# Kernel tuning notes

Measured on AMD Instinct MI355X. Metric: run time of the kernel, lower is better.

Reference implementation:

```python
import jax, jax.numpy as jnp
import numpy as np

N = 100000      # nodes
E = 3200000     # edges
G = 256         # graphs in batch
EPS = 1e-5      # BatchNorm eps


def gcn_conv(x, W, b, src, dst, norm):
    # x: [N, Fin] -> [N, Fout]. PyG GCNConv: linear, then sym-normalized
    # scatter-add over edges (self-loops already included in src/dst/norm).
    h = x @ W                                   # [N, Fout]
    msg = h[src] * norm[:, None]                # [E+N, Fout] gather + scale
    out = jax.ops.segment_sum(msg, dst, num_segments=N)
    return out + b


def bn_eval(x, gamma, beta, rm, rv):
    return (x - rm) * jax.lax.rsqrt(rv + EPS) * gamma + beta


def setup_inputs() -> dict:
    key = jax.random.key(0)
    ks = jax.random.split(key, 24)
    x = jax.random.normal(ks[0], (N, 8), dtype=jnp.float32)
    edge_index = jax.random.randint(ks[1], (2, E), 0, N, dtype=jnp.int64)
    batch = jnp.sort(jax.random.randint(ks[2], (N,), 0, G, dtype=jnp.int64))

    def lin(k, fin, fout):
        return jax.random.normal(k, (fin, fout), dtype=jnp.float32) / np.sqrt(fin)

    d = {
        "x": x, "edge_index": edge_index, "batch": batch,
        "W1": lin(ks[3], 8, 64),  "b1": jnp.zeros((64,), jnp.float32),
        "g1": jnp.ones((64,), jnp.float32), "be1": jnp.zeros((64,), jnp.float32),
        "rm1": jax.random.normal(ks[4], (64,), jnp.float32) * 0.1,
        "rv1": jnp.ones((64,), jnp.float32) + jax.random.uniform(ks[5], (64,)) * 0.1,
        "W2": lin(ks[6], 64, 64), "b2": jnp.zeros((64,), jnp.float32),
        "g2": jnp.ones((64,), jnp.float32), "be2": jnp.zeros((64,), jnp.float32),
        "rm2": jax.random.normal(ks[7], (64,), jnp.float32) * 0.1,
        "rv2": jnp.ones((64,), jnp.float32) + jax.random.uniform(ks[8], (64,)) * 0.1,
        "W3": lin(ks[9], 64, 64), "b3": jnp.zeros((64,), jnp.float32),
        "g3": jnp.ones((64,), jnp.float32), "be3": jnp.zeros((64,), jnp.float32),
        "rm3": jax.random.normal(ks[10], (64,), jnp.float32) * 0.1,
        "rv3": jnp.ones((64,), jnp.float32) + jax.random.uniform(ks[11], (64,)) * 0.1,
        "Wr1": lin(ks[12], 64, 64), "br1": jnp.zeros((64,), jnp.float32),
        "Wr2": lin(ks[13], 64, 2),  "br2": jnp.zeros((2,), jnp.float32),
    }
    return d


def reference(x, edge_index, batch,
              W1, b1, g1, be1, rm1, rv1,
              W2, b2, g2, be2, rm2, rv2,
              W3, b3, g3, be3, rm3, rv3,
              Wr1, br1, Wr2, br2):
    # add self-loops once; compute symmetric normalization deg^-1/2
    loops = jnp.arange(N, dtype=edge_index.dtype)
    src = jnp.concatenate([edge_index[0], loops])   # [E+N]
    dst = jnp.concatenate([edge_index[1], loops])
    deg = jax.ops.segment_sum(jnp.ones_like(dst, dtype=x.dtype), dst, num_segments=N)
    dinv = jnp.where(deg > 0, jax.lax.rsqrt(deg), 0.0)
    norm = dinv[src] * dinv[dst]                    # [E+N]

    h = jax.nn.relu(bn_eval(gcn_conv(x, W1, b1, src, dst, norm), g1, be1, rm1, rv1))
    h = jax.nn.relu(bn_eval(gcn_conv(h, W2, b2, src, dst, norm), g2, be2, rm2, rv2))
    h = jax.nn.relu(bn_eval(gcn_conv(h, W3, b3, src, dst, norm), g3, be3, rm3, rv3))

    # global mean pool over graph ids
    sums = jax.ops.segment_sum(h, batch, num_segments=G)           # [G, 64]
    cnts = jax.ops.segment_sum(jnp.ones((N,), h.dtype), batch, num_segments=G)
    pooled = sums / jnp.maximum(cnts, 1.0)[:, None]

    out = jax.nn.relu(pooled @ Wr1 + br1) @ Wr2 + br2              # [G, 2]
    return out
```

## Files before the change

### kernel.cpp

```cpp
#include <hip/hip_runtime.h>
#include <hip/hip_fp16.h>

#define NN 100000
#define NE 3200000
#define NG 256
#define NF (NN * 64)
#define FEPS 1e-5f
#define BSH 8
#define NB ((NN + 255) >> 8)
#define CHA 8192

static inline int ceil_div(int a, int b) { return (a + b - 1) / b; }


__global__ __launch_bounds__(256) void kA_hist(const int* __restrict__ dst,
                                               int* __restrict__ bh) {
    __shared__ int lh[NB];
    int t = threadIdx.x;
    for (int b = t; b < NB; b += 256) lh[b] = 0;
    __syncthreads();
    int e0 = blockIdx.x * CHA;
    int e1 = min(e0 + CHA, NE);
    for (int i = e0 + t; i < e1; i += 256) atomicAdd(&lh[dst[i] >> BSH], 1);
    __syncthreads();
    for (int b = t; b < NB; b += 256)
        if (lh[b]) atomicAdd(&bh[b], lh[b]);
}

__global__ __launch_bounds__(512) void kA_scan(const int* __restrict__ bh,
                                               int* __restrict__ bboff,
                                               int* __restrict__ bcur) {
    __shared__ int s[512];
    int t = threadIdx.x;
    int v = (t < NB) ? bh[t] : 0;
    s[t] = v;
    __syncthreads();
    for (int off = 1; off < 512; off <<= 1) {
        int add = (t >= off) ? s[t - off] : 0;
        __syncthreads();
        s[t] += add;
        __syncthreads();
    }
    if (t < NB) {
        int ex = s[t] - v;
        bboff[t] = ex;
        bcur[t] = ex;
    }
    if (t == 0) bboff[NB] = NE;
}

__global__ __launch_bounds__(256) void kA_fill(const int* __restrict__ src,
                                               const int* __restrict__ dst,
                                               int* __restrict__ bcur,
                                               int2* __restrict__ ebuf) {
    __shared__ int lh[NB];
    __shared__ int lbase[NB];
    __shared__ int lcur[NB];
    int t = threadIdx.x;
    for (int b = t; b < NB; b += 256) lh[b] = 0;
    __syncthreads();
    int e0 = blockIdx.x * CHA;
    int e1 = min(e0 + CHA, NE);
    for (int i = e0 + t; i < e1; i += 256) atomicAdd(&lh[dst[i] >> BSH], 1);
    __syncthreads();
    for (int b = t; b < NB; b += 256) {
        int c = lh[b];
        lbase[b] = c ? atomicAdd(&bcur[b], c) : 0;
        lcur[b] = 0;
    }
    __syncthreads();
    for (int i = e0 + t; i < e1; i += 256) {
        int d = dst[i];
        int s = src[i];
        int b = d >> BSH;
        int p = atomicAdd(&lcur[b], 1);
        ebuf[lbase[b] + p] = make_int2(s, d);
    }
}


__global__ __launch_bounds__(256) void kB_hist(const int2* __restrict__ ebuf,
                                               const int* __restrict__ bboff,
                                               int* __restrict__ cnt) {
    __shared__ int lc[256];
    int b = blockIdx.x;
    int t = threadIdx.x;
    lc[t] = 0;
    __syncthreads();
    int st = bboff[b], en = bboff[b + 1];
    for (int i = st + t; i < en; i += 256) atomicAdd(&lc[ebuf[i].y & 255], 1);
    __syncthreads();
    int node = (b << BSH) + t;
    if (node < NN) cnt[node] = lc[t];
}

__global__ __launch_bounds__(256) void k_dinv_xs(const int* __restrict__ cnt,
                                                 const float* __restrict__ x,
                                                 float* __restrict__ dinv,
                                                 __half* __restrict__ xs) {
    int i = blockIdx.x * 256 + threadIdx.x;
    if (i >= NN) return;
    float di = rsqrtf((float)cnt[i] + 1.0f);
    dinv[i] = di;
#pragma unroll
    for (int f = 0; f < 8; ++f) xs[i * 8 + f] = __float2half(x[i * 8 + f] * di);
}

__global__ __launch_bounds__(256) void k_scan1(const int* __restrict__ cnt,
                                               int* __restrict__ bsum) {
    __shared__ int s[256];
    int t = threadIdx.x;
    int i = blockIdx.x * 256 + t;
    s[t] = (i < NN) ? cnt[i] : 0;
    __syncthreads();
    for (int off = 128; off > 0; off >>= 1) {
        if (t < off) s[t] += s[t + off];
        __syncthreads();
    }
    if (t == 0) bsum[blockIdx.x] = s[0];
}

__global__ __launch_bounds__(512) void k_scan2(int* __restrict__ bsum, int nb) {
    __shared__ int s[512];
    int t = threadIdx.x;
    int v = (t < nb) ? bsum[t] : 0;
    s[t] = v;
    __syncthreads();
    for (int off = 1; off < 512; off <<= 1) {
        int add = (t >= off) ? s[t - off] : 0;
        __syncthreads();
        s[t] += add;
        __syncthreads();
    }
    if (t < nb) bsum[t] = s[t] - v;
}

__global__ __launch_bounds__(256) void k_scan3(const int* __restrict__ cnt,
                                               const int* __restrict__ bsum,
                                               int* __restrict__ rowptr) {
    __shared__ int s[256];
    int t = threadIdx.x;
    int i = blockIdx.x * 256 + t;
    int v = (i < NN) ? cnt[i] : 0;
    s[t] = v;
    __syncthreads();
    for (int off = 1; off < 256; off <<= 1) {
        int add = (t >= off) ? s[t - off] : 0;
        __syncthreads();
        s[t] += add;
        __syncthreads();
    }
    if (i < NN) rowptr[i] = s[t] - v + bsum[blockIdx.x];
}

__global__ __launch_bounds__(256) void kB_fill(const int2* __restrict__ ebuf,
                                               const int* __restrict__ bboff,
                                               const int* __restrict__ rowptr,
                                               int* __restrict__ csr) {
    __shared__ int rp[256];
    __shared__ int lc[256];
    int b = blockIdx.x;
    int t = threadIdx.x;
    int node = (b << BSH) + t;
    rp[t] = (node < NN) ? rowptr[node] : 0;
    lc[t] = 0;
    __syncthreads();
    int st = bboff[b], en = bboff[b + 1];
    for (int i = st + t; i < en; i += 256) {
        int2 e = ebuf[i];
        int dl = e.y & 255;
        int p = atomicAdd(&lc[dl], 1);
        csr[rp[dl] + p] = e.x;
    }
}


__global__ __launch_bounds__(256) void k_gxf8(const __half* __restrict__ xs,
                                              const int* __restrict__ rowptr,
                                              const int* __restrict__ cnt,
                                              const float* __restrict__ dinv,
                                              const int* __restrict__ csr,
                                              const float* __restrict__ W,
                                              const float* __restrict__ b,
                                              const float* __restrict__ g,
                                              const float* __restrict__ be,
                                              const float* __restrict__ rm,
                                              const float* __restrict__ rv,
                                              __half* __restrict__ out) {
    __shared__ float Ws[512];
    int tid = threadIdx.x;
    for (int i = tid; i < 512; i += 256) Ws[i] = W[i];
    __syncthreads();
    int wave = (blockIdx.x * 256 + tid) >> 6;
    int lane = tid & 63;
    if (wave >= NN) return;
    int es = lane >> 3, f = lane & 7;
    int st = rowptr[wave], n = cnt[wave];
    float acc = 0.f;
    for (int k0 = 0; k0 < n; k0 += 8) {
        int kk = k0 + es;
        if (kk < n) acc += __half2float(xs[csr[st + kk] * 8 + f]);
    }
    acc += __shfl_xor(acc, 8, 64);
    acc += __shfl_xor(acc, 16, 64);
    acc += __shfl_xor(acc, 32, 64);
    float di = dinv[wave];
    float pf = (acc + __half2float(xs[wave * 8 + f])) * di;
    float scale = g[lane] * rsqrtf(rv[lane] + FEPS);
    float shift = be[lane] + (b[lane] - rm[lane]) * scale;
    float o = 0.f;
#pragma unroll
    for (int k = 0; k < 8; ++k)
        o = fmaf(__shfl(pf, k, 64), Ws[k * 64 + lane], o);
    o = fmaxf(fmaf(o, scale, shift), 0.f);
    out[wave * 64 + lane] = __float2half(o * di);
}

template <bool SCALE_OUT>
__global__ __launch_bounds__(256) void k_gxf64(const __half* __restrict__ Hin,
                                               const int* __restrict__ rowptr,
                                               const int* __restrict__ cnt,
                                               const float* __restrict__ dinv,
                                               const int* __restrict__ csr,
                                               const float* __restrict__ W,
                                               const float* __restrict__ b,
                                               const float* __restrict__ g,
                                               const float* __restrict__ be,
                                               const float* __restrict__ rm,
                                               const float* __restrict__ rv,
                                               __half* __restrict__ out) {
    __shared__ float Ws[4096];
    int tid = threadIdx.x;
    for (int i = tid; i < 4096; i += 256) Ws[i] = W[i];
    __syncthreads();
    int wave = (blockIdx.x * 256 + tid) >> 6;
    int lane = tid & 63;
    if (wave >= NN) return;
    int st = rowptr[wave], n = cnt[wave];
    float a0 = __half2float(Hin[wave * 64 + lane]);
    float a1 = 0.f;
    int k = 0;
    while (k < n) {
        int rem = n - k;
        int chunk = rem < 64 ? rem : 64;
        int eidx = (lane < chunk) ? csr[st + k + lane] : 0;
        int j = 0;
        for (; j + 8 <= chunk; j += 8) {
            int s0 = __shfl(eidx, j + 0, 64);
            int s1 = __shfl(eidx, j + 1, 64);
            int s2 = __shfl(eidx, j + 2, 64);
            int s3 = __shfl(eidx, j + 3, 64);
            int s4 = __shfl(eidx, j + 4, 64);
            int s5 = __shfl(eidx, j + 5, 64);
            int s6 = __shfl(eidx, j + 6, 64);
            int s7 = __shfl(eidx, j + 7, 64);
            float v0 = __half2float(Hin[s0 * 64 + lane]);
            float v1 = __half2float(Hin[s1 * 64 + lane]);
            float v2 = __half2float(Hin[s2 * 64 + lane]);
            float v3 = __half2float(Hin[s3 * 64 + lane]);
            float v4 = __half2float(Hin[s4 * 64 + lane]);
            float v5 = __half2float(Hin[s5 * 64 + lane]);
            float v6 = __half2float(Hin[s6 * 64 + lane]);
            float v7 = __half2float(Hin[s7 * 64 + lane]);
            a0 += (v0 + v1) + (v2 + v3);
            a1 += (v4 + v5) + (v6 + v7);
        }
        for (; j < chunk; ++j) {
            int s = __shfl(eidx, j, 64);
            a0 += __half2float(Hin[s * 64 + lane]);
        }
        k += chunk;
    }
    float di = dinv[wave];
    float pf = (a0 + a1) * di;
    float scale = g[lane] * rsqrtf(rv[lane] + FEPS);
    float shift = be[lane] + (b[lane] - rm[lane]) * scale;
    float o0 = 0.f, o1 = 0.f, o2 = 0.f, o3 = 0.f;
#pragma unroll
    for (int k2 = 0; k2 < 64; k2 += 4) {
        o0 = fmaf(__shfl(pf, k2 + 0, 64), Ws[(k2 + 0) * 64 + lane], o0);
        o1 = fmaf(__shfl(pf, k2 + 1, 64), Ws[(k2 + 1) * 64 + lane], o1);
        o2 = fmaf(__shfl(pf, k2 + 2, 64), Ws[(k2 + 2) * 64 + lane], o2);
        o3 = fmaf(__shfl(pf, k2 + 3, 64), Ws[(k2 + 3) * 64 + lane], o3);
    }
    float o = (o0 + o1) + (o2 + o3);
    o = fmaxf(fmaf(o, scale, shift), 0.f);
    if (SCALE_OUT) o *= di;
    out[wave * 64 + lane] = __float2half(o);
}


__global__ __launch_bounds__(256) void k_pool(const __half* __restrict__ h,
                                              const int* __restrict__ batch,
                                              float* __restrict__ sums,
                                              float* __restrict__ cnts) {
    const int CHUNK = 32;
    int gw = (blockIdx.x * 256 + threadIdx.x) >> 6;
    int lane = threadIdx.x & 63;
    int nw = (gridDim.x * 256) >> 6;
    int nchunks = (NN + CHUNK - 1) / CHUNK;
    for (int c = gw; c < nchunks; c += nw) {
        int n0 = c * CHUNK;
        int n1 = min(n0 + CHUNK, NN);
        int gcur = batch[n0];
        float accf = 0.f;
        float cntf = 0.f;
        for (int n = n0; n < n1; ++n) {
            int gg = batch[n];
            if (gg != gcur) {
                atomicAdd(&sums[gcur * 64 + lane], accf);
                if (lane == 0) atomicAdd(&cnts[gcur], cntf);
                accf = 0.f;
                cntf = 0.f;
                gcur = gg;
            }
            accf += __half2float(h[n * 64 + lane]);
            cntf += 1.f;
        }
        atomicAdd(&sums[gcur * 64 + lane], accf);
        if (lane == 0) atomicAdd(&cnts[gcur], cntf);
    }
}

__global__ __launch_bounds__(256) void k_head(const float* __restrict__ sums,
                                              const float* __restrict__ cnts,
                                              const float* __restrict__ Wr1,
                                              const float* __restrict__ br1,
                                              const float* __restrict__ Wr2,
                                              const float* __restrict__ br2,
                                              float* __restrict__ out) {
    int wave = (blockIdx.x * 256 + threadIdx.x) >> 6;
    int lane = threadIdx.x & 63;
    if (wave >= NG) return;
    float c = fmaxf(cnts[wave], 1.0f);
    float pooled = sums[wave * 64 + lane] / c;
    float acc = 0.f;
#pragma unroll
    for (int k = 0; k < 64; ++k)
        acc = fmaf(__shfl(pooled, k, 64), Wr1[k * 64 + lane], acc);
    float hid = fmaxf(acc + br1[lane], 0.f);
    float o0 = hid * Wr2[lane * 2 + 0];
    float o1 = hid * Wr2[lane * 2 + 1];
#pragma unroll
    for (int off = 32; off > 0; off >>= 1) {
        o0 += __shfl_xor(o0, off, 64);
        o1 += __shfl_xor(o1, off, 64);
    }
    if (lane == 0) {
        out[wave * 2 + 0] = o0 + br2[0];
        out[wave * 2 + 1] = o1 + br2[1];
    }
}

extern "C" void kernel_launch(void* const* d_in, const int* in_sizes, int n_in,
                              void* d_out, int out_size, void* d_ws, size_t ws_size,
                              hipStream_t stream) {
    const float* x   = (const float*)d_in[0];
    const int*   ei  = (const int*)d_in[1];
    const int*   bat = (const int*)d_in[2];
    const float* W1  = (const float*)d_in[3];
    const float* b1  = (const float*)d_in[4];
    const float* g1  = (const float*)d_in[5];
    const float* be1 = (const float*)d_in[6];
    const float* rm1 = (const float*)d_in[7];
    const float* rv1 = (const float*)d_in[8];
    const float* W2  = (const float*)d_in[9];
    const float* b2  = (const float*)d_in[10];
    const float* g2  = (const float*)d_in[11];
    const float* be2 = (const float*)d_in[12];
    const float* rm2 = (const float*)d_in[13];
    const float* rv2 = (const float*)d_in[14];
    const float* W3  = (const float*)d_in[15];
    const float* b3  = (const float*)d_in[16];
    const float* g3  = (const float*)d_in[17];
    const float* be3 = (const float*)d_in[18];
    const float* rm3 = (const float*)d_in[19];
    const float* rv3 = (const float*)d_in[20];
    const float* Wr1 = (const float*)d_in[21];
    const float* br1 = (const float*)d_in[22];
    const float* Wr2 = (const float*)d_in[23];
    const float* br2 = (const float*)d_in[24];
    float* out = (float*)d_out;

    int*    cnt    = (int*)d_ws;
    int*    rowptr = cnt + NN;
    int*    bsum   = rowptr + NN;
    int*    bh     = bsum + 512;
    int*    bboff  = bh + NB;
    int*    bcur   = bboff + NB + 1;
    float*  dinv   = (float*)(bcur + NB);
    int*    csr    = (int*)(dinv + NN);
    __half* xs     = (__half*)(csr + NE);
    float*  sums   = (float*)(xs + NN * 8);
    float*  cnts   = sums + NG * 64;
    __half* A      = (__half*)(cnts + NG);
    __half* B      = A + NF;
    int2*   ebuf   = (int2*)A;

    const int* srcI = ei;
    const int* dstI = ei + NE;

    const int gA = ceil_div(NE, CHA);
    const int gN = ceil_div(NN, 256);
    const int gW = ceil_div(NN * 64, 256);

    hipMemsetAsync(bh, 0, NB * sizeof(int), stream);
    hipMemsetAsync(sums, 0, (NG * 64 + NG) * sizeof(float), stream);

    kA_hist<<<gA, 256, 0, stream>>>(dstI, bh);
    kA_scan<<<1, 512, 0, stream>>>(bh, bboff, bcur);
    kA_fill<<<gA, 256, 0, stream>>>(srcI, dstI, bcur, ebuf);

    kB_hist<<<NB, 256, 0, stream>>>(ebuf, bboff, cnt);
    k_dinv_xs<<<gN, 256, 0, stream>>>(cnt, x, dinv, xs);
    k_scan1<<<gN, 256, 0, stream>>>(cnt, bsum);
    k_scan2<<<1, 512, 0, stream>>>(bsum, gN);
    k_scan3<<<gN, 256, 0, stream>>>(cnt, bsum, rowptr);
    kB_fill<<<NB, 256, 0, stream>>>(ebuf, bboff, rowptr, csr);

    k_gxf8<<<gW, 256, 0, stream>>>(xs, rowptr, cnt, dinv, csr,
                                   W1, b1, g1, be1, rm1, rv1, A);
    k_gxf64<true><<<gW, 256, 0, stream>>>(A, rowptr, cnt, dinv, csr,
                                          W2, b2, g2, be2, rm2, rv2, B);
    k_gxf64<false><<<gW, 256, 0, stream>>>(B, rowptr, cnt, dinv, csr,
                                           W3, b3, g3, be3, rm3, rv3, A);

    k_pool<<<800, 256, 0, stream>>>(A, bat, sums, cnts);
    k_head<<<ceil_div(NG * 64, 256), 256, 0, stream>>>(sums, cnts, Wr1, br1, Wr2, br2, out);
}
```

Baseline: 648.6 us.

## Vectorize neighbor gathers with half2 and fuse mean-pool into last GCN layer

The layer-1 and layer-2/3 aggregation kernels now load two fp16 features per lane as half2. Each wave load instruction covers two neighbor rows (half-waves split the edges), and a final cross-half shuffle reduces the two halves. This halves the number of gather instructions on the bandwidth-bound aggregation. The separate pooling kernel is removed. The last layer now atomically adds each node's output straight into per-graph sums, and node counts come from a small new kernel. This skips writing and re-reading the final activations, but adds one float atomic per feature per node onto only 256×64 addresses, so contention is a risk.

Measured after the change: 619.8 us. 4.4% less time.

```diff
diff --git a/kernel.cpp b/kernel.cpp
--- a/kernel.cpp
+++ b/kernel.cpp
@@ -174,8 +174,28 @@
     }
 }
 
-
-__global__ __launch_bounds__(256) void k_gxf8(const __half* __restrict__ xs,
+__global__ __launch_bounds__(256) void k_cnts(const int* __restrict__ batch,
+                                              float* __restrict__ cnts) {
+    int c = blockIdx.x * 256 + threadIdx.x;
+    int n0 = c * 64;
+    if (n0 >= NN) return;
+    int n1 = min(n0 + 64, NN);
+    int gcur = batch[n0];
+    float cf = 0.f;
+    for (int n = n0; n < n1; ++n) {
+        int gg = batch[n];
+        if (gg != gcur) {
+            atomicAdd(&cnts[gcur], cf);
+            cf = 0.f;
+            gcur = gg;
+        }
+        cf += 1.f;
+    }
+    atomicAdd(&cnts[gcur], cf);
+}
+
+
+__global__ __launch_bounds__(256) void k_gxf8(const __half2* __restrict__ xs2,
                                               const int* __restrict__ rowptr,
                                               const int* __restrict__ cnt,
                                               const float* __restrict__ dinv,
@@ -194,30 +214,40 @@
     int wave = (blockIdx.x * 256 + tid) >> 6;
     int lane = tid & 63;
     if (wave >= NN) return;
-    int es = lane >> 3, f = lane & 7;
+    int es = lane >> 2, q = lane & 3;
     int st = rowptr[wave], n = cnt[wave];
-    float acc = 0.f;
-    for (int k0 = 0; k0 < n; k0 += 8) {
+    float ax = 0.f, ay = 0.f;
+    for (int k0 = 0; k0 < n; k0 += 16) {
         int kk = k0 + es;
-        if (kk < n) acc += __half2float(xs[csr[st + kk] * 8 + f]);
-    }
-    acc += __shfl_xor(acc, 8, 64);
-    acc += __shfl_xor(acc, 16, 64);
-    acc += __shfl_xor(acc, 32, 64);
+        if (kk < n) {
+            float2 f = __half22float2(xs2[csr[st + kk] * 4 + q]);
+            ax += f.x; ay += f.y;
+        }
+    }
+    ax += __shfl_xor(ax, 4, 64);  ay += __shfl_xor(ay, 4, 64);
+    ax += __shfl_xor(ax, 8, 64);  ay += __shfl_xor(ay, 8, 64);
+    ax += __shfl_xor(ax, 16, 64); ay += __shfl_xor(ay, 16, 64);
+    ax += __shfl_xor(ax, 32, 64); ay += __shfl_xor(ay, 32, 64);
     float di = dinv[wave];
-    float pf = (acc + __half2float(xs[wave * 8 + f])) * di;
+    float2 s2 = __half22float2(xs2[wave * 4 + q]);
+    float pfx = (ax + s2.x) * di;
+    float pfy = (ay + s2.y) * di;
     float scale = g[lane] * rsqrtf(rv[lane] + FEPS);
     float shift = be[lane] + (b[lane] - rm[lane]) * scale;
     float o = 0.f;
 #pragma unroll
-    for (int k = 0; k < 8; ++k)
-        o = fmaf(__shfl(pf, k, 64), Ws[k * 64 + lane], o);
+    for (int qq = 0; qq < 4; ++qq) {
+        float vx = __shfl(pfx, qq, 64);
+        float vy = __shfl(pfy, qq, 64);
+        o = fmaf(vx, Ws[(2 * qq) * 64 + lane], o);
+        o = fmaf(vy, Ws[(2 * qq + 1) * 64 + lane], o);
+    }
     o = fmaxf(fmaf(o, scale, shift), 0.f);
     out[wave * 64 + lane] = __float2half(o * di);
 }
 
-template <bool SCALE_OUT>
-__global__ __launch_bounds__(256) void k_gxf64(const __half* __restrict__ Hin,
+template <bool POOL>
+__global__ __launch_bounds__(256) void k_gxf64(const __half2* __restrict__ Hin2,
                                                const int* __restrict__ rowptr,
                                                const int* __restrict__ cnt,
                                                const float* __restrict__ dinv,
@@ -228,7 +258,9 @@
                                                const float* __restrict__ be,
                                                const float* __restrict__ rm,
                                                const float* __restrict__ rv,
-                                               __half* __restrict__ out) {
+                                               const int* __restrict__ batch,
+                                               __half* __restrict__ out,
+                                               float* __restrict__ sums) {
     __shared__ float Ws[4096];
     int tid = threadIdx.x;
     for (int i = tid; i < 4096; i += 256) Ws[i] = W[i];
@@ -236,91 +268,76 @@
     int wave = (blockIdx.x * 256 + tid) >> 6;
     int lane = tid & 63;
     if (wave >= NN) return;
+    int p = lane >> 5;
+    int q = lane & 31;
     int st = rowptr[wave], n = cnt[wave];
-    float a0 = __half2float(Hin[wave * 64 + lane]);
-    float a1 = 0.f;
+    float ax = 0.f, ay = 0.f;
     int k = 0;
     while (k < n) {
         int rem = n - k;
         int chunk = rem < 64 ? rem : 64;
         int eidx = (lane < chunk) ? csr[st + k + lane] : 0;
         int j = 0;
-        for (; j + 8 <= chunk; j += 8) {
-            int s0 = __shfl(eidx, j + 0, 64);
-            int s1 = __shfl(eidx, j + 1, 64);
-            int s2 = __shfl(eidx, j + 2, 64);
-            int s3 = __shfl(eidx, j + 3, 64);
-            int s4 = __shfl(eidx, j + 4, 64);
-            int s5 = __shfl(eidx, j + 5, 64);
-            int s6 = __shfl(eidx, j + 6, 64);
-            int s7 = __shfl(eidx, j + 7, 64);
-            float v0 = __half2float(Hin[s0 * 64 + lane]);
-            float v1 = __half2float(Hin[s1 * 64 + lane]);
-            float v2 = __half2float(Hin[s2 * 64 + lane]);
-            float v3 = __half2float(Hin[s3 * 64 + lane]);
-            float v4 = __half2float(Hin[s4 * 64 + lane]);
-            float v5 = __half2float(Hin[s5 * 64 + lane]);
-            float v6 = __half2float(Hin[s6 * 64 + lane]);
-            float v7 = __half2float(Hin[s7 * 64 + lane]);
-            a0 += (v0 + v1) + (v2 + v3);
-            a1 += (v4 + v5) + (v6 + v7);
+        for (; j + 16 <= chunk; j += 16) {
+            int s0 = __shfl(eidx, j + 0 + p, 64);
+            int s1 = __shfl(eidx, j + 2 + p, 64);
+            int s2 = __shfl(eidx, j + 4 + p, 64);
+            int s3 = __shfl(eidx, j + 6 + p, 64);
+            int s4 = __shfl(eidx, j + 8 + p, 64);
+            int s5 = __shfl(eidx, j + 10 + p, 64);
+            int s6 = __shfl(eidx, j + 12 + p, 64);
+            int s7 = __shfl(eidx, j + 14 + p, 64);
+            float2 f0 = __half22float2(Hin2[s0 * 32 + q]);
+            float2 f1 = __half22float2(Hin2[s1 * 32 + q]);
+            float2 f2 = __half22float2(Hin2[s2 * 32 + q]);
+            float2 f3 = __half22float2(Hin2[s3 * 32 + q]);
+            float2 f4 = __half22float2(Hin2[s4 * 32 + q]);
+            float2 f5 = __half22float2(Hin2[s5 * 32 + q]);
+            float2 f6 = __half22float2(Hin2[s6 * 32 + q]);
+            float2 f7 = __half22float2(Hin2[s7 * 32 + q]);
+            ax += ((f0.x + f1.x) + (f2.x + f3.x)) + ((f4.x + f5.x) + (f6.x + f7.x));
+            ay += ((f0.y + f1.y) + (f2.y + f3.y)) + ((f4.y + f5.y) + (f6.y + f7.y));
         }
-        for (; j < chunk; ++j) {
+        for (; j + 2 <= chunk; j += 2) {
+            int s = __shfl(eidx, j + p, 64);
+            float2 f = __half22float2(Hin2[s * 32 + q]);
+            ax += f.x; ay += f.y;
+        }
+        if (j < chunk) {
             int s = __shfl(eidx, j, 64);
-            a0 += __half2float(Hin[s * 64 + lane]);
+            if (p == 0) {
+                float2 f = __half22float2(Hin2[s * 32 + q]);
+                ax += f.x; ay += f.y;
+            }
         }
         k += chunk;
     }
+    ax += __shfl_xor(ax, 32, 64);
+    ay += __shfl_xor(ay, 32, 64);
     float di = dinv[wave];
-    float pf = (a0 + a1) * di;
+    float2 s2 = __half22float2(Hin2[wave * 32 + q]);
+    float pfx = (ax + s2.x) * di;
+    float pfy = (ay + s2.y) * di;
     float scale = g[lane] * rsqrtf(rv[lane] + FEPS);
     float shift = be[lane] + (b[lane] - rm[lane]) * scale;
-    float o0 = 0.f, o1 = 0.f, o2 = 0.f, o3 = 0.f;
+    float o0 = 0.f, o1 = 0.f;
 #pragma unroll
-    for (int k2 = 0; k2 < 64; k2 += 4) {
-        o0 = fmaf(__shfl(pf, k2 + 0, 64), Ws[(k2 + 0) * 64 + lane], o0);
-        o1 = fmaf(__shfl(pf, k2 + 1, 64), Ws[(k2 + 1) * 64 + lane], o1);
-        o2 = fmaf(__shfl(pf, k2 + 2, 64), Ws[(k2 + 2) * 64 + lane], o2);
-        o3 = fmaf(__shfl(pf, k2 + 3, 64), Ws[(k2 + 3) * 64 + lane], o3);
-    }
-    float o = (o0 + o1) + (o2 + o3);
+    for (int qq = 0; qq < 32; ++qq) {
+        float vx = __shfl(pfx, qq, 64);
+        float vy = __shfl(pfy, qq, 64);
+        o0 = fmaf(vx, Ws[(2 * qq) * 64 + lane], o0);
+        o1 = fmaf(vy, Ws[(2 * qq + 1) * 64 + lane], o1);
+    }
+    float o = o0 + o1;
     o = fmaxf(fmaf(o, scale, shift), 0.f);
-    if (SCALE_OUT) o *= di;
-    out[wave * 64 + lane] = __float2half(o);
-}
-
-
-__global__ __launch_bounds__(256) void k_pool(const __half* __restrict__ h,
-                                              const int* __restrict__ batch,
-                                              float* __restrict__ sums,
-                                              float* __restrict__ cnts) {
-    const int CHUNK = 32;
-    int gw = (blockIdx.x * 256 + threadIdx.x) >> 6;
-    int lane = threadIdx.x & 63;
-    int nw = (gridDim.x * 256) >> 6;
-    int nchunks = (NN + CHUNK - 1) / CHUNK;
-    for (int c = gw; c < nchunks; c += nw) {
-        int n0 = c * CHUNK;
-        int n1 = min(n0 + CHUNK, NN);
-        int gcur = batch[n0];
-        float accf = 0.f;
-        float cntf = 0.f;
-        for (int n = n0; n < n1; ++n) {
-            int gg = batch[n];
-            if (gg != gcur) {
-                atomicAdd(&sums[gcur * 64 + lane], accf);
-                if (lane == 0) atomicAdd(&cnts[gcur], cntf);
-                accf = 0.f;
-                cntf = 0.f;
-                gcur = gg;
-            }
-            accf += __half2float(h[n * 64 + lane]);
-            cntf += 1.f;
-        }
-        atomicAdd(&sums[gcur * 64 + lane], accf);
-        if (lane == 0) atomicAdd(&cnts[gcur], cntf);
-    }
-}
+    if (POOL) {
+        int gg = batch[wave];
+        atomicAdd(&sums[gg * 64 + lane], o);
+    } else {
+        out[wave * 64 + lane] = __float2half(o * di);
+    }
+}
+
 
 __global__ __launch_bounds__(256) void k_head(const float* __restrict__ sums,
                                               const float* __restrict__ cnts,
@@ -413,18 +430,20 @@
 
     kB_hist<<<NB, 256, 0, stream>>>(ebuf, bboff, cnt);
     k_dinv_xs<<<gN, 256, 0, stream>>>(cnt, x, dinv, xs);
+    k_cnts<<<ceil_div(ceil_div(NN, 64), 256), 256, 0, stream>>>(bat, cnts);
     k_scan1<<<gN, 256, 0, stream>>>(cnt, bsum);
     k_scan2<<<1, 512, 0, stream>>>(bsum, gN);
     k_scan3<<<gN, 256, 0, stream>>>(cnt, bsum, rowptr);
     kB_fill<<<NB, 256, 0, stream>>>(ebuf, bboff, rowptr, csr);
 
-    k_gxf8<<<gW, 256, 0, stream>>>(xs, rowptr, cnt, dinv, csr,
+    k_gxf8<<<gW, 256, 0, stream>>>((const __half2*)xs, rowptr, cnt, dinv, csr,
                                    W1, b1, g1, be1, rm1, rv1, A);
-    k_gxf64<true><<<gW, 256, 0, stream>>>(A, rowptr, cnt, dinv, csr,
-                                          W2, b2, g2, be2, rm2, rv2, B);
-    k_gxf64<false><<<gW, 256, 0, stream>>>(B, rowptr, cnt, dinv, csr,
-                                           W3, b3, g3, be3, rm3, rv3, A);
-
-    k_pool<<<800, 256, 0, stream>>>(A, bat, sums, cnts);
+    k_gxf64<false><<<gW, 256, 0, stream>>>((const __half2*)A, rowptr, cnt, dinv, csr,
+                                           W2, b2, g2, be2, rm2, rv2,
+                                           bat, B, nullptr);
+    k_gxf64<true><<<gW, 256, 0, stream>>>((const __half2*)B, rowptr, cnt, dinv, csr,
+                                          W3, b3, g3, be3, rm3, rv3,
+                                          bat, nullptr, sums);
+
     k_head<<<ceil_div(NG * 64, 256), 256, 0, stream>>>(sums, cnts, Wr1, br1, Wr2, br2, out);
 }
```
